# Performance work log

Measured on AMD Instinct MI355X. Metric: run time of the kernel, lower is better.

The kernel has to match this reference:

```python
import jax, jax.numpy as jnp
import numpy as np

# Sobel kernels stacked as 2 output channels of a 1-input-channel 3x3 conv: [2,1,3,3]
_SOBEL = jnp.array([
    [[[-1., 0., 1.], [-2., 0., 2.], [-1., 0., 1.]]],   # sobel_x
    [[[-1., -2., -1.], [0., 0., 0.], [1., 2., 1.]]],   # sobel_y
], dtype=jnp.float32)


def _edge_map(x):
    # x: [B, C, H, W] -> per-class edge magnitude |Gx| + |Gy|, same shape.
    B, C, H, W = x.shape
    xr = x.reshape(B * C, 1, H, W)  # fold classes into batch: one fused conv
    g = jax.lax.conv_general_dilated(
        xr, _SOBEL.astype(x.dtype),
        window_strides=(1, 1), padding=((1, 1), (1, 1)),
        dimension_numbers=("NCHW", "OIHW", "NCHW"))  # [B*C, 2, H, W]
    e = jnp.abs(g[:, 0]) + jnp.abs(g[:, 1])           # [B*C, H, W]
    return e.reshape(B, C, H, W)


def setup_inputs() -> dict:
    key = jax.random.key(0)
    k1, k2 = jax.random.split(key)
    B, C, H, W = 16, 19, 512, 512
    inputs = jax.random.normal(k1, (B, C, H, W), dtype=jnp.float32)
    targets = jax.random.randint(k2, (B, H, W), 0, C, dtype=jnp.int64)
    return {"inputs": inputs, "targets": targets}


def reference(inputs, targets):
    C = inputs.shape[1]
    targets_one_hot = jax.nn.one_hot(targets, C, axis=1, dtype=inputs.dtype)  # [B,C,H,W]
    edge_in = _edge_map(inputs)
    edge_tg = _edge_map(targets_one_hot)
    # F.mse_loss per class (mean over B,H,W) then summed over classes.
    sq = (edge_in - edge_tg) ** 2
    per_class = jnp.mean(sq, axis=(0, 2, 3))  # [C]
    return jnp.sum(per_class)
```

## Files before the change

### kernel.cpp

```cpp
#include <hip/hip_runtime.h>

namespace {
constexpr int B = 16, C = 19, H = 512, W = 512;
constexpr int TPB = 256;
constexpr int H_CHUNK = 128;
constexpr int NWB = W / TPB;
constexpr int NHC = H / H_CHUNK;
constexpr int NXCD = 8;
constexpr int TILES = B * NHC * NWB;
constexpr int TILES_PER_XCD = TILES / NXCD;
constexpr int TOTAL_BLOCKS = TILES * C;
constexpr float SCALE = 1.0f / (float)((long long)B * H * W);
}

__global__ void zero_out_kernel(float* out) { *out = 0.0f; }

__global__ __launch_bounds__(TPB) void edge_loss_kernel(
    const float* __restrict__ X,
    const int*   __restrict__ T,
    float* __restrict__ out)
{
    int i = (int)blockIdx.x;
    const int xcd  = i & (NXCD - 1);
    const int j    = i >> 3;
    const int c    = j % C;
    const int tl   = j / C;
    const int tile = xcd * TILES_PER_XCD + tl;
    const int wb   = tile & 1;
    const int hc   = (tile >> 1) & 3;
    const int b    = tile >> 3;

    const int tid = (int)threadIdx.x;
    const int w   = wb * TPB + tid;
    const int h0  = hc * H_CHUNK;

    const float* __restrict__ Xs = X + (size_t)(b * C + c) * (size_t)(H * W);
    const int*   __restrict__ Ts = T + (size_t)b * (size_t)(H * W);

    const int   wm = (w > 0)     ? (w - 1) : 0;
    const int   wp = (w < W - 1) ? (w + 1) : (W - 1);
    const float fl = (w > 0)     ? 1.0f : 0.0f;
    const float fr = (w < W - 1) ? 1.0f : 0.0f;

    const float* xr = Xs + (size_t)h0 * W;
    const int*   tr = Ts + (size_t)h0 * W;

    auto ldrow = [&](const float* xrow, const int* trow,
                     float& d, float& s, float& e, float& u) {
        const float xm = xrow[wm] * fl;
        const float x0 = xrow[w];
        const float xp = xrow[wp] * fr;
        const int   ta = trow[wm];
        const int   t0 = trow[w];
        const int   tb = trow[wp];
        const float mm = (ta == c) ? fl : 0.0f;
        const float m0 = (t0 == c) ? 1.0f : 0.0f;
        const float mp = (tb == c) ? fr : 0.0f;
        d = xp - xm;
        s = fmaf(2.0f, x0, xm + xp);
        e = mp - mm;
        u = fmaf(2.0f, m0, mm + mp);
    };

    float d0,s0,e0,u0, d1,s1,e1,u1, d2,s2,e2,u2;
    float acc = 0.0f;

#define COMPUTE(dA,sA,eA,uA, dB,sB,eB,uB, dC,sC,eC,uC)          \
    {                                                           \
        const float gx = fmaf(2.0f, dB, dA + dC);               \
        const float gy = sC - sA;                               \
        const float hx = fmaf(2.0f, eB, eA + eC);               \
        const float hy = uC - uA;                               \
        const float dd = (fabsf(gx) + fabsf(gy))                \
                       - (fabsf(hx) + fabsf(hy));               \
        acc = fmaf(dd, dd, acc);                                \
    }
#define BODY(dA,sA,eA,uA, dB,sB,eB,uB, dC,sC,eC,uC)             \
    {                                                           \
        xr += W; tr += W;                                       \
        ldrow(xr, tr, dC, sC, eC, uC);                          \
        COMPUTE(dA,sA,eA,uA, dB,sB,eB,uB, dC,sC,eC,uC)          \
    }

    if (hc == 0) { d0 = s0 = e0 = u0 = 0.0f; }
    else         ldrow(xr - W, tr - W, d0, s0, e0, u0);
    ldrow(xr, tr, d1, s1, e1, u1);

    for (int t = 0; t < 42; ++t) {
        BODY(d0,s0,e0,u0, d1,s1,e1,u1, d2,s2,e2,u2)
        BODY(d1,s1,e1,u1, d2,s2,e2,u2, d0,s0,e0,u0)
        BODY(d2,s2,e2,u2, d0,s0,e0,u0, d1,s1,e1,u1)
    }
    BODY(d0,s0,e0,u0, d1,s1,e1,u1, d2,s2,e2,u2)
    if (hc == NHC - 1) { d0 = s0 = e0 = u0 = 0.0f; }
    else { xr += W; tr += W; ldrow(xr, tr, d0, s0, e0, u0); }
    COMPUTE(d1,s1,e1,u1, d2,s2,e2,u2, d0,s0,e0,u0)

#undef BODY
#undef COMPUTE

    #pragma unroll
    for (int off = 32; off > 0; off >>= 1)
        acc += __shfl_down(acc, off, 64);

    __shared__ float wsum[TPB / 64];
    const int lane = tid & 63;
    const int wid  = tid >> 6;
    if (lane == 0) wsum[wid] = acc;
    __syncthreads();
    if (tid == 0)
        atomicAdd(out, (wsum[0] + wsum[1] + wsum[2] + wsum[3]) * SCALE);
}

extern "C" void kernel_launch(void* const* d_in, const int* in_sizes, int n_in,
                              void* d_out, int out_size, void* d_ws, size_t ws_size,
                              hipStream_t stream) {
    (void)in_sizes; (void)n_in; (void)d_ws; (void)ws_size; (void)out_size;
    const float* X = (const float*)d_in[0];
    const int*   T = (const int*)d_in[1];
    float* out = (float*)d_out;

    zero_out_kernel<<<1, 1, 0, stream>>>(out);
    edge_loss_kernel<<<TOTAL_BLOCKS, TPB, 0, stream>>>(X, T, out);
}
```

Baseline: 109.5 us.

## Process four columns per thread with software-pipelined row loads and shorter row chunks

Each thread now handles four adjacent columns of a full 512-wide row, using 128-thread blocks and 32-row chunks instead of one column per thread over 128 rows. Row loads are double-buffered so the next row's loads are issued before the current row is aggregated. The intent is fewer redundant neighbour loads, more memory-level parallelism per thread, and more blocks for better occupancy. In exchange, halo rows are reloaded more often and register pressure rises. The loads are unaligned scalar loads, so they may not vectorise.

```diff
diff --git a/kernel.cpp b/kernel.cpp
--- a/kernel.cpp
+++ b/kernel.cpp
@@ -2,16 +2,21 @@
 
 namespace {
 constexpr int B = 16, C = 19, H = 512, W = 512;
-constexpr int TPB = 256;
-constexpr int H_CHUNK = 128;
-constexpr int NWB = W / TPB;
-constexpr int NHC = H / H_CHUNK;
+constexpr int TPB = 128;
+constexpr int HC = 32;
+constexpr int NHC = H / HC;
 constexpr int NXCD = 8;
-constexpr int TILES = B * NHC * NWB;
-constexpr int TILES_PER_XCD = TILES / NXCD;
-constexpr int TOTAL_BLOCKS = TILES * C;
+constexpr int TILES = B * NHC;
+constexpr int TPX = TILES / NXCD;
+constexpr int NBLK = TILES * C;
 constexpr float SCALE = 1.0f / (float)((long long)B * H * W);
 }
+
+struct Raw {
+    float xa0, xa1, xa2, xa3, xb0, xb1;
+    int   ta0, ta1, ta2, ta3, tb0, tb1;
+};
+struct Agg { float d0,d1,d2,d3, s0,s1,s2,s3, e0,e1,e2,e3, u0,u1,u2,u3; };
 
 __global__ void zero_out_kernel(float* out) { *out = 0.0f; }
 
@@ -25,91 +30,133 @@
     const int j    = i >> 3;
     const int c    = j % C;
     const int tl   = j / C;
-    const int tile = xcd * TILES_PER_XCD + tl;
-    const int wb   = tile & 1;
-    const int hc   = (tile >> 1) & 3;
-    const int b    = tile >> 3;
+    const int tile = xcd * TPX + tl;
+    const int b    = tile >> 4;
+    const int hc   = tile & (NHC - 1);
+    const int h0   = hc * HC;
 
-    const int tid = (int)threadIdx.x;
-    const int w   = wb * TPB + tid;
-    const int h0  = hc * H_CHUNK;
+    const int tid  = (int)threadIdx.x;
+    const int w0   = tid << 2;
+    const bool imgL = (tid == 0);
+    const bool imgR = (tid == TPB - 1);
+    const int colA = imgL ? 0 : (w0 - 1);
+    const int colB = imgR ? (w0 + 2) : (w0 + 3);
 
     const float* __restrict__ Xs = X + (size_t)(b * C + c) * (size_t)(H * W);
     const int*   __restrict__ Ts = T + (size_t)b * (size_t)(H * W);
 
-    const int   wm = (w > 0)     ? (w - 1) : 0;
-    const int   wp = (w < W - 1) ? (w + 1) : (W - 1);
-    const float fl = (w > 0)     ? 1.0f : 0.0f;
-    const float fr = (w < W - 1) ? 1.0f : 0.0f;
+    const int r0 = (hc == 0) ? 0 : (h0 - 1);
+    const float* pxa = Xs + (size_t)r0 * W + colA;
+    const float* pxb = Xs + (size_t)r0 * W + colB;
+    const int*   pta = Ts + (size_t)r0 * W + colA;
+    const int*   ptb = Ts + (size_t)r0 * W + colB;
+    const int step1 = (hc == 0) ? 0 : W;
 
-    const float* xr = Xs + (size_t)h0 * W;
-    const int*   tr = Ts + (size_t)h0 * W;
+    auto issue = [&](Raw& q) {
+        q.xa0 = pxa[0]; q.xa1 = pxa[1]; q.xa2 = pxa[2]; q.xa3 = pxa[3];
+        q.xb0 = pxb[0]; q.xb1 = pxb[1];
+        q.ta0 = pta[0]; q.ta1 = pta[1]; q.ta2 = pta[2]; q.ta3 = pta[3];
+        q.tb0 = ptb[0]; q.tb1 = ptb[1];
+    };
+    auto advance = [&](int dw) { pxa += dw; pxb += dw; pta += dw; ptb += dw; };
 
-    auto ldrow = [&](const float* xrow, const int* trow,
-                     float& d, float& s, float& e, float& u) {
-        const float xm = xrow[wm] * fl;
-        const float x0 = xrow[w];
-        const float xp = xrow[wp] * fr;
-        const int   ta = trow[wm];
-        const int   t0 = trow[w];
-        const int   tb = trow[wp];
-        const float mm = (ta == c) ? fl : 0.0f;
-        const float m0 = (t0 == c) ? 1.0f : 0.0f;
-        const float mp = (tb == c) ? fr : 0.0f;
-        d = xp - xm;
-        s = fmaf(2.0f, x0, xm + xp);
-        e = mp - mm;
-        u = fmaf(2.0f, m0, mm + mp);
+    auto aggregate = [&](Agg& g, const Raw& q) {
+        const float xm = imgL ? 0.f   : q.xa0;
+        const float x0 = imgL ? q.xa0 : q.xa1;
+        const float x1 = imgL ? q.xa1 : q.xa2;
+        const float x2 = imgL ? q.xa2 : q.xa3;
+        const float x3 = imgR ? q.xb1 : q.xb0;
+        const float xp = imgR ? 0.f   : q.xb1;
+        const float nA = (q.ta0 == c) ? 1.f : 0.f;
+        const float nB = (q.ta1 == c) ? 1.f : 0.f;
+        const float nC = (q.ta2 == c) ? 1.f : 0.f;
+        const float nD = (q.ta3 == c) ? 1.f : 0.f;
+        const float nE = (q.tb0 == c) ? 1.f : 0.f;
+        const float nF = (q.tb1 == c) ? 1.f : 0.f;
+        const float mm = imgL ? 0.f : nA;
+        const float m0 = imgL ? nA  : nB;
+        const float m1 = imgL ? nB  : nC;
+        const float m2 = imgL ? nC  : nD;
+        const float m3 = imgR ? nF  : nE;
+        const float mp = imgR ? 0.f : nF;
+        g.d0 = x1 - xm; g.d1 = x2 - x0; g.d2 = x3 - x1; g.d3 = xp - x2;
+        g.s0 = fmaf(2.f, x0, xm + x1); g.s1 = fmaf(2.f, x1, x0 + x2);
+        g.s2 = fmaf(2.f, x2, x1 + x3); g.s3 = fmaf(2.f, x3, x2 + xp);
+        g.e0 = m1 - mm; g.e1 = m2 - m0; g.e2 = m3 - m1; g.e3 = mp - m2;
+        g.u0 = fmaf(2.f, m0, mm + m1); g.u1 = fmaf(2.f, m1, m0 + m2);
+        g.u2 = fmaf(2.f, m2, m1 + m3); g.u3 = fmaf(2.f, m3, m2 + mp);
+    };
+    auto zagg = [&](Agg& g) {
+        g.d0=g.d1=g.d2=g.d3 = g.s0=g.s1=g.s2=g.s3 =
+        g.e0=g.e1=g.e2=g.e3 = g.u0=g.u1=g.u2=g.u3 = 0.f;
     };
 
-    float d0,s0,e0,u0, d1,s1,e1,u1, d2,s2,e2,u2;
-    float acc = 0.0f;
+    float ac0 = 0.f, ac1 = 0.f, ac2 = 0.f, ac3 = 0.f;
+    auto comp = [&](const Agg& A, const Agg& Bb, const Agg& Cc) {
+#define CM(k) {                                                     \
+        const float gx = fmaf(2.f, Bb.d##k, A.d##k + Cc.d##k);      \
+        const float gy = Cc.s##k - A.s##k;                          \
+        const float hx = fmaf(2.f, Bb.e##k, A.e##k + Cc.e##k);      \
+        const float hy = Cc.u##k - A.u##k;                          \
+        const float dd = (fabsf(gx) + fabsf(gy))                    \
+                       - (fabsf(hx) + fabsf(hy));                   \
+        ac##k = fmaf(dd, dd, ac##k); }
+        CM(0) CM(1) CM(2) CM(3)
+#undef CM
+    };
 
-#define COMPUTE(dA,sA,eA,uA, dB,sB,eB,uB, dC,sC,eC,uC)          \
-    {                                                           \
-        const float gx = fmaf(2.0f, dB, dA + dC);               \
-        const float gy = sC - sA;                               \
-        const float hx = fmaf(2.0f, eB, eA + eC);               \
-        const float hy = uC - uA;                               \
-        const float dd = (fabsf(gx) + fabsf(gy))                \
-                       - (fabsf(hx) + fabsf(hy));               \
-        acc = fmaf(dd, dd, acc);                                \
+    Raw qa, qb;
+    Agg g0, g1, g2;
+
+    issue(qa);
+    advance(step1);
+    issue(qb);
+    advance(W);
+    aggregate(g0, qa);
+    if (hc == 0) zagg(g0);
+    issue(qa);
+    advance(W);
+    aggregate(g1, qb);
+
+#define PSTEP(QI, QC, GA, GB, GC) \
+    issue(QI); advance(W);        \
+    aggregate(GC, QC);            \
+    comp(GA, GB, GC);
+
+    for (int t6 = 0; t6 < 5; ++t6) {
+        PSTEP(qb, qa, g0, g1, g2)
+        PSTEP(qa, qb, g1, g2, g0)
+        PSTEP(qb, qa, g2, g0, g1)
+        PSTEP(qa, qb, g0, g1, g2)
+        PSTEP(qb, qa, g1, g2, g0)
+        PSTEP(qa, qb, g2, g0, g1)
     }
-#define BODY(dA,sA,eA,uA, dB,sB,eB,uB, dC,sC,eC,uC)             \
-    {                                                           \
-        xr += W; tr += W;                                       \
-        ldrow(xr, tr, dC, sC, eC, uC);                          \
-        COMPUTE(dA,sA,eA,uA, dB,sB,eB,uB, dC,sC,eC,uC)          \
+#undef PSTEP
+
+    {
+        const int back = (hc == NHC - 1) ? W : 0;
+        pxa -= back; pxb -= back; pta -= back; ptb -= back;
+        issue(qb);
+        aggregate(g2, qa);
+        comp(g0, g1, g2);
+    }
+    {
+        aggregate(g0, qb);
+        if (hc == NHC - 1) zagg(g0);
+        comp(g1, g2, g0);
     }
 
-    if (hc == 0) { d0 = s0 = e0 = u0 = 0.0f; }
-    else         ldrow(xr - W, tr - W, d0, s0, e0, u0);
-    ldrow(xr, tr, d1, s1, e1, u1);
-
-    for (int t = 0; t < 42; ++t) {
-        BODY(d0,s0,e0,u0, d1,s1,e1,u1, d2,s2,e2,u2)
-        BODY(d1,s1,e1,u1, d2,s2,e2,u2, d0,s0,e0,u0)
-        BODY(d2,s2,e2,u2, d0,s0,e0,u0, d1,s1,e1,u1)
-    }
-    BODY(d0,s0,e0,u0, d1,s1,e1,u1, d2,s2,e2,u2)
-    if (hc == NHC - 1) { d0 = s0 = e0 = u0 = 0.0f; }
-    else { xr += W; tr += W; ldrow(xr, tr, d0, s0, e0, u0); }
-    COMPUTE(d1,s1,e1,u1, d2,s2,e2,u2, d0,s0,e0,u0)
-
-#undef BODY
-#undef COMPUTE
-
+    float a = (ac0 + ac1) + (ac2 + ac3);
     #pragma unroll
     for (int off = 32; off > 0; off >>= 1)
-        acc += __shfl_down(acc, off, 64);
+        a += __shfl_down(a, off, 64);
 
     __shared__ float wsum[TPB / 64];
     const int lane = tid & 63;
     const int wid  = tid >> 6;
-    if (lane == 0) wsum[wid] = acc;
+    if (lane == 0) wsum[wid] = a;
     __syncthreads();
-    if (tid == 0)
-        atomicAdd(out, (wsum[0] + wsum[1] + wsum[2] + wsum[3]) * SCALE);
+    if (tid == 0) atomicAdd(out, (wsum[0] + wsum[1]) * SCALE);
 }
 
 extern "C" void kernel_launch(void* const* d_in, const int* in_sizes, int n_in,
@@ -121,5 +168,5 @@
     float* out = (float*)d_out;
 
     zero_out_kernel<<<1, 1, 0, stream>>>(out);
-    edge_loss_kernel<<<TOTAL_BLOCKS, TPB, 0, stream>>>(X, T, out);
+    edge_loss_kernel<<<NBLK, TPB, 0, stream>>>(X, T, out);
 }
```

After: 110.4 us. About the same (+0.8%).

## Vectorize row loads to float4/int4 with 4 columns per thread and prefetch

Applied to the files above, without the earlier changes.

Each thread now handles four adjacent columns using float4/int4 loads plus two scalar halo loads, instead of three scalar loads per row. Blocks shrink to 128 threads covering a full 512-wide row, and the row chunk drops from 128 to 32, giving more blocks. Row loads are issued one row ahead of the computation as a software pipeline. The aim is fewer load instructions and more memory-level parallelism in this bandwidth-bound stencil, at the cost of more registers and more redundant halo rows across the smaller chunks.

```diff
diff --git a/kernel.cpp b/kernel.cpp
--- a/kernel.cpp
+++ b/kernel.cpp
@@ -2,20 +2,22 @@
 
 namespace {
 constexpr int B = 16, C = 19, H = 512, W = 512;
-constexpr int TPB = 256;
-constexpr int H_CHUNK = 128;
-constexpr int NWB = W / TPB;
-constexpr int NHC = H / H_CHUNK;
+constexpr int TPB = 128;
+constexpr int HC = 32;
+constexpr int NHC = H / HC;
 constexpr int NXCD = 8;
-constexpr int TILES = B * NHC * NWB;
-constexpr int TILES_PER_XCD = TILES / NXCD;
-constexpr int TOTAL_BLOCKS = TILES * C;
+constexpr int TILES = B * NHC;
+constexpr int TPX = TILES / NXCD;
+constexpr int NBLK = TILES * C;
 constexpr float SCALE = 1.0f / (float)((long long)B * H * W);
 }
 
+struct Raw { float4 x; float xl, xr; int4 t; int tl, tr; };
+struct Agg { float4 d, s, e, u; };
+
 __global__ void zero_out_kernel(float* out) { *out = 0.0f; }
 
-__global__ __launch_bounds__(TPB) void edge_loss_kernel(
+__global__ __launch_bounds__(TPB, 4) void edge_loss_kernel(
     const float* __restrict__ X,
     const int*   __restrict__ T,
     float* __restrict__ out)
@@ -24,92 +26,142 @@
     const int xcd  = i & (NXCD - 1);
     const int j    = i >> 3;
     const int c    = j % C;
-    const int tl   = j / C;
-    const int tile = xcd * TILES_PER_XCD + tl;
-    const int wb   = tile & 1;
-    const int hc   = (tile >> 1) & 3;
-    const int b    = tile >> 3;
+    const int tl_  = j / C;
+    const int tile = xcd * TPX + tl_;
+    const int b    = tile >> 4;
+    const int hc   = tile & (NHC - 1);
+    const int h0   = hc * HC;
 
     const int tid = (int)threadIdx.x;
-    const int w   = wb * TPB + tid;
-    const int h0  = hc * H_CHUNK;
+    const int w0  = tid << 2;
+    const int   colL = (w0 > 0)     ? (w0 - 1) : 0;
+    const int   colR = (w0 + 4 < W) ? (w0 + 4) : (W - 1);
+    const float fl   = (w0 > 0)     ? 1.0f : 0.0f;
+    const float fr   = (w0 + 4 < W) ? 1.0f : 0.0f;
 
     const float* __restrict__ Xs = X + (size_t)(b * C + c) * (size_t)(H * W);
     const int*   __restrict__ Ts = T + (size_t)b * (size_t)(H * W);
 
-    const int   wm = (w > 0)     ? (w - 1) : 0;
-    const int   wp = (w < W - 1) ? (w + 1) : (W - 1);
-    const float fl = (w > 0)     ? 1.0f : 0.0f;
-    const float fr = (w < W - 1) ? 1.0f : 0.0f;
+    const int r0 = (hc == 0) ? 0 : (h0 - 1);
+    const int step1 = (hc == 0) ? 0 : W;
+    const float* xb = Xs + (size_t)r0 * W;
+    const int*   tb = Ts + (size_t)r0 * W;
 
-    const float* xr = Xs + (size_t)h0 * W;
-    const int*   tr = Ts + (size_t)h0 * W;
+    Raw q0, q1, q2;
+    Agg ga, gb, gc;
+    float ac0 = 0.f, ac1 = 0.f, ac2 = 0.f, ac3 = 0.f;
 
-    auto ldrow = [&](const float* xrow, const int* trow,
-                     float& d, float& s, float& e, float& u) {
-        const float xm = xrow[wm] * fl;
-        const float x0 = xrow[w];
-        const float xp = xrow[wp] * fr;
-        const int   ta = trow[wm];
-        const int   t0 = trow[w];
-        const int   tb = trow[wp];
-        const float mm = (ta == c) ? fl : 0.0f;
-        const float m0 = (t0 == c) ? 1.0f : 0.0f;
-        const float mp = (tb == c) ? fr : 0.0f;
-        d = xp - xm;
-        s = fmaf(2.0f, x0, xm + xp);
-        e = mp - mm;
-        u = fmaf(2.0f, m0, mm + mp);
-    };
-
-    float d0,s0,e0,u0, d1,s1,e1,u1, d2,s2,e2,u2;
-    float acc = 0.0f;
-
-#define COMPUTE(dA,sA,eA,uA, dB,sB,eB,uB, dC,sC,eC,uC)          \
-    {                                                           \
-        const float gx = fmaf(2.0f, dB, dA + dC);               \
-        const float gy = sC - sA;                               \
-        const float hx = fmaf(2.0f, eB, eA + eC);               \
-        const float hy = uC - uA;                               \
-        const float dd = (fabsf(gx) + fabsf(gy))                \
-                       - (fabsf(hx) + fabsf(hy));               \
-        acc = fmaf(dd, dd, acc);                                \
-    }
-#define BODY(dA,sA,eA,uA, dB,sB,eB,uB, dC,sC,eC,uC)             \
-    {                                                           \
-        xr += W; tr += W;                                       \
-        ldrow(xr, tr, dC, sC, eC, uC);                          \
-        COMPUTE(dA,sA,eA,uA, dB,sB,eB,uB, dC,sC,eC,uC)          \
+#define ISSUE(Q)                                                     \
+    {                                                                \
+        (Q).x  = *reinterpret_cast<const float4*>(xb + w0);          \
+        (Q).xl = xb[colL]; (Q).xr = xb[colR];                        \
+        (Q).t  = *reinterpret_cast<const int4*>(tb + w0);            \
+        (Q).tl = tb[colL]; (Q).tr = tb[colR];                        \
+        xb += W; tb += W;                                            \
     }
 
-    if (hc == 0) { d0 = s0 = e0 = u0 = 0.0f; }
-    else         ldrow(xr - W, tr - W, d0, s0, e0, u0);
-    ldrow(xr, tr, d1, s1, e1, u1);
+#define AGG(G, Q)                                                    \
+    {                                                                \
+        const float xm = (Q).xl * fl;                                \
+        const float xp = (Q).xr * fr;                                \
+        const float m0 = ((Q).t.x == c) ? 1.f : 0.f;                 \
+        const float m1 = ((Q).t.y == c) ? 1.f : 0.f;                 \
+        const float m2 = ((Q).t.z == c) ? 1.f : 0.f;                 \
+        const float m3 = ((Q).t.w == c) ? 1.f : 0.f;                 \
+        const float mm = ((Q).tl  == c) ? fl  : 0.f;                 \
+        const float mp = ((Q).tr  == c) ? fr  : 0.f;                 \
+        (G).d.x = (Q).x.y - xm;      (G).d.y = (Q).x.z - (Q).x.x;    \
+        (G).d.z = (Q).x.w - (Q).x.y; (G).d.w = xp - (Q).x.z;         \
+        (G).s.x = fmaf(2.f, (Q).x.x, xm + (Q).x.y);                  \
+        (G).s.y = fmaf(2.f, (Q).x.y, (Q).x.x + (Q).x.z);             \
+        (G).s.z = fmaf(2.f, (Q).x.z, (Q).x.y + (Q).x.w);             \
+        (G).s.w = fmaf(2.f, (Q).x.w, (Q).x.z + xp);                  \
+        (G).e.x = m1 - mm; (G).e.y = m2 - m0;                        \
+        (G).e.z = m3 - m1; (G).e.w = mp - m2;                        \
+        (G).u.x = fmaf(2.f, m0, mm + m1);                            \
+        (G).u.y = fmaf(2.f, m1, m0 + m2);                            \
+        (G).u.z = fmaf(2.f, m2, m1 + m3);                            \
+        (G).u.w = fmaf(2.f, m3, m2 + mp);                            \
+    }
 
-    for (int t = 0; t < 42; ++t) {
-        BODY(d0,s0,e0,u0, d1,s1,e1,u1, d2,s2,e2,u2)
-        BODY(d1,s1,e1,u1, d2,s2,e2,u2, d0,s0,e0,u0)
-        BODY(d2,s2,e2,u2, d0,s0,e0,u0, d1,s1,e1,u1)
+#define ZAGG(G)                                                      \
+    (G).d = (G).s = (G).e = (G).u = make_float4(0.f, 0.f, 0.f, 0.f);
+
+#define COMP(A, Bb, Cc)                                              \
+    {                                                                \
+        float gx, gy, hx, hy, dd;                                    \
+        gx = fmaf(2.f, (Bb).d.x, (A).d.x + (Cc).d.x);                \
+        gy = (Cc).s.x - (A).s.x;                                     \
+        hx = fmaf(2.f, (Bb).e.x, (A).e.x + (Cc).e.x);                \
+        hy = (Cc).u.x - (A).u.x;                                     \
+        dd = (fabsf(gx) + fabsf(gy)) - (fabsf(hx) + fabsf(hy));      \
+        ac0 = fmaf(dd, dd, ac0);                                     \
+        gx = fmaf(2.f, (Bb).d.y, (A).d.y + (Cc).d.y);                \
+        gy = (Cc).s.y - (A).s.y;                                     \
+        hx = fmaf(2.f, (Bb).e.y, (A).e.y + (Cc).e.y);                \
+        hy = (Cc).u.y - (A).u.y;                                     \
+        dd = (fabsf(gx) + fabsf(gy)) - (fabsf(hx) + fabsf(hy));      \
+        ac1 = fmaf(dd, dd, ac1);                                     \
+        gx = fmaf(2.f, (Bb).d.z, (A).d.z + (Cc).d.z);                \
+        gy = (Cc).s.z - (A).s.z;                                     \
+        hx = fmaf(2.f, (Bb).e.z, (A).e.z + (Cc).e.z);                \
+        hy = (Cc).u.z - (A).u.z;                                     \
+        dd = (fabsf(gx) + fabsf(gy)) - (fabsf(hx) + fabsf(hy));      \
+        ac2 = fmaf(dd, dd, ac2);                                     \
+        gx = fmaf(2.f, (Bb).d.w, (A).d.w + (Cc).d.w);                \
+        gy = (Cc).s.w - (A).s.w;                                     \
+        hx = fmaf(2.f, (Bb).e.w, (A).e.w + (Cc).e.w);                \
+        hy = (Cc).u.w - (A).u.w;                                     \
+        dd = (fabsf(gx) + fabsf(gy)) - (fabsf(hx) + fabsf(hy));      \
+        ac3 = fmaf(dd, dd, ac3);                                     \
     }
-    BODY(d0,s0,e0,u0, d1,s1,e1,u1, d2,s2,e2,u2)
-    if (hc == NHC - 1) { d0 = s0 = e0 = u0 = 0.0f; }
-    else { xr += W; tr += W; ldrow(xr, tr, d0, s0, e0, u0); }
-    COMPUTE(d1,s1,e1,u1, d2,s2,e2,u2, d0,s0,e0,u0)
 
-#undef BODY
-#undef COMPUTE
+    {
+        ISSUE(q0);
+        xb += (step1 - W); tb += (step1 - W);
+        ISSUE(q1);
+        ISSUE(q2);
+    }
+    AGG(ga, q0);
+    if (hc == 0) { ZAGG(ga); }
+    ISSUE(q0);
+    AGG(gb, q1);
 
+    for (int t3 = 0; t3 < 9; ++t3) {
+        ISSUE(q1); AGG(gc, q2); COMP(ga, gb, gc);
+        ISSUE(q2); AGG(ga, q0); COMP(gb, gc, ga);
+        ISSUE(q0); AGG(gb, q1); COMP(gc, ga, gb);
+    }
+    ISSUE(q1); AGG(gc, q2); COMP(ga, gb, gc);
+    ISSUE(q2); AGG(ga, q0); COMP(gb, gc, ga);
+
+    {
+        const int back = (hc == NHC - 1) ? W : 0;
+        xb -= back; tb -= back;
+        ISSUE(q0);
+        AGG(gb, q1); COMP(gc, ga, gb);
+    }
+    AGG(gc, q2); COMP(ga, gb, gc);
+    AGG(ga, q0);
+    if (hc == NHC - 1) { ZAGG(ga); }
+    COMP(gb, gc, ga);
+
+#undef ISSUE
+#undef AGG
+#undef ZAGG
+#undef COMP
+
+    float a = (ac0 + ac1) + (ac2 + ac3);
     #pragma unroll
     for (int off = 32; off > 0; off >>= 1)
-        acc += __shfl_down(acc, off, 64);
+        a += __shfl_down(a, off, 64);
 
     __shared__ float wsum[TPB / 64];
     const int lane = tid & 63;
     const int wid  = tid >> 6;
-    if (lane == 0) wsum[wid] = acc;
+    if (lane == 0) wsum[wid] = a;
     __syncthreads();
-    if (tid == 0)
-        atomicAdd(out, (wsum[0] + wsum[1] + wsum[2] + wsum[3]) * SCALE);
+    if (tid == 0) atomicAdd(out, (wsum[0] + wsum[1]) * SCALE);
 }
 
 extern "C" void kernel_launch(void* const* d_in, const int* in_sizes, int n_in,
@@ -121,5 +173,5 @@
     float* out = (float*)d_out;
 
     zero_out_kernel<<<1, 1, 0, stream>>>(out);
-    edge_loss_kernel<<<TOTAL_BLOCKS, TPB, 0, stream>>>(X, T, out);
+    edge_loss_kernel<<<NBLK, TPB, 0, stream>>>(X, T, out);
 }
```

Result: slower. 129.8 us (+18.5%).
